# Optimization experiments

Measured on AMD Instinct MI355X. Metric: run time of the kernel, lower is better.

Reference implementation:

```python
import jax, jax.numpy as jnp
import numpy as np

N, E, IN_DIM, EDGE_DIM, EMB, H, L = 50000, 800000, 128, 32, 256, 8, 4
C = EMB // H  # per-head channels = 32
NEG_SLOPE = 0.2


def setup_inputs() -> dict:
    key = jax.random.key(0)
    ks = jax.random.split(key, 12)
    s = lambda d: 1.0 / np.sqrt(d)
    return {
        "x": jax.random.normal(ks[0], (N, IN_DIM), jnp.float32),
        "edge_index": jax.random.randint(ks[1], (2, E), 0, N, jnp.int32),
        "edge_attr": jax.random.normal(ks[2], (E, EDGE_DIM), jnp.float32),
        "w_in": jax.random.normal(ks[3], (IN_DIM, EMB), jnp.float32) * s(IN_DIM),
        "b_in": jnp.zeros((EMB,), jnp.float32),
        "W_l": jax.random.normal(ks[4], (L, EMB, EMB), jnp.float32) * s(EMB),
        "We_l": jax.random.normal(ks[5], (L, EDGE_DIM, EMB), jnp.float32) * s(EDGE_DIM),
        "att_src": jax.random.normal(ks[6], (L, H, C), jnp.float32) * s(C),
        "att_dst": jax.random.normal(ks[7], (L, H, C), jnp.float32) * s(C),
        "att_edge": jax.random.normal(ks[8], (L, H, C), jnp.float32) * s(C),
        "bias_l": jnp.zeros((L, EMB), jnp.float32),
        "w_out": jax.random.normal(ks[9], (EMB, 1), jnp.float32) * s(EMB),
        "b_out": jnp.zeros((1,), jnp.float32),
    }


def _gat_forward(x, edge_index, edge_attr, w_in, b_in, W_l, We_l,
                 att_src, att_dst, att_edge, bias_l, w_out, b_out):
    # add self loops (PyG GATConv default, edge_attr fill_value='mean')
    loop = jnp.arange(N, dtype=edge_index.dtype)
    src = jnp.concatenate([edge_index[0], loop])  # [E+N]
    dst = jnp.concatenate([edge_index[1], loop])
    ea = jnp.concatenate([edge_attr,
                          jnp.broadcast_to(edge_attr.mean(0), (N, EDGE_DIM))], 0)

    h = x @ w_in + b_in  # [N, EMB]
    for l in range(L):
        hp = (h @ W_l[l]).reshape(N, H, C)            # [N,H,C]
        ep = (ea @ We_l[l]).reshape(-1, H, C)         # [E+N,H,C]
        a_s = (hp * att_src[l]).sum(-1)               # [N,H]
        a_d = (hp * att_dst[l]).sum(-1)               # [N,H]
        e = a_s[src] + a_d[dst] + (ep * att_edge[l]).sum(-1)  # [E+N,H]
        e = jnp.where(e >= 0, e, NEG_SLOPE * e)
        # segment softmax over incoming edges of each dst node
        m = jax.ops.segment_max(e, dst, num_segments=N)
        e = jnp.exp(e - m[dst])
        denom = jax.ops.segment_sum(e, dst, num_segments=N)
        alpha = e / (denom[dst] + 1e-16)              # [E+N,H]
        msg = hp[src] * alpha[..., None]              # [E+N,H,C]
        h = jax.ops.segment_sum(msg, dst, num_segments=N).reshape(N, EMB) + bias_l[l]
    out = h @ w_out + b_out                           # [N,1]
    return out.squeeze(1)


def reference(x, edge_index, edge_attr, w_in, b_in, W_l, We_l,
              att_src, att_dst, att_edge, bias_l, w_out, b_out):
    return _gat_forward(x, edge_index, edge_attr, w_in, b_in, W_l, We_l,
                        att_src, att_dst, att_edge, bias_l, w_out, b_out)
```

## Files before the change

### kernel.cpp

```cpp
#include <hip/hip_runtime.h>

#define NN 50000
#define MPAD 50048
#define EE 800000
#define ETOT (EE + NN)
#define IN_DIM 128
#define EDGE_DIM 32
#define EMB 256
#define HH 8
#define LL 4
#define NEG_SLOPE 0.2f

typedef __attribute__((ext_vector_type(8))) short bf16x8;
typedef __attribute__((ext_vector_type(4))) float f32x4;

__device__ inline ushort f2bf_rn(float x) {
    union { float f; uint u; } v; v.f = x;
    uint r = v.u + 0x7FFFu + ((v.u >> 16) & 1u);
    return (ushort)(r >> 16);
}
__device__ inline float bf2f(ushort b) {
    union { uint u; float f; } v; v.u = ((uint)b) << 16;
    return v.f;
}

__device__ __forceinline__ void g2l16(const void* g, void* l) {
    __builtin_amdgcn_global_load_lds((const __attribute__((address_space(1))) void*)g,
                                     (__attribute__((address_space(3))) void*)l, 16, 0, 0);
}


__global__ void zero_int_kernel(int* p, int n) {
    int i = blockIdx.x * 256 + threadIdx.x;
    if (i < n) p[i] = 0;
}

__global__ void precompute_kernel(const float* __restrict__ We,
                                  const float* __restrict__ att_e,
                                  float* __restrict__ v) {
    int t = threadIdx.x;
    int l = t >> 8, rem = t & 255, d = rem >> 3, hh = rem & 7;
    float s = 0.f;
#pragma unroll
    for (int c = 0; c < 32; ++c)
        s += We[((size_t)(l * 32 + d)) * 256 + hh * 32 + c] * att_e[l * 256 + hh * 32 + c];
    v[t] = s;
}

__global__ __launch_bounds__(256) void col_partial(const float* __restrict__ ea,
                                                   float* __restrict__ part) {
    int t = threadIdx.x;
    int c = t & 7;
    int rg = t >> 3;
    float4 acc = {0.f, 0.f, 0.f, 0.f};
    for (int r = blockIdx.x * 32 + rg; r < EE; r += 1024 * 32) {
        float4 f = *(const float4*)&ea[(size_t)r * 32 + c * 4];
        acc.x += f.x; acc.y += f.y; acc.z += f.z; acc.w += f.w;
    }
    __shared__ float4 sm[256];
    sm[t] = acc;
    __syncthreads();
    for (int s = 16; s > 0; s >>= 1) {
        if (rg < s) {
            float4 o = sm[(rg + s) * 8 + c];
            float4 m = sm[t];
            m.x += o.x; m.y += o.y; m.z += o.z; m.w += o.w;
            sm[t] = m;
        }
        __syncthreads();
    }
    if (t < 8) *(float4*)&part[(size_t)blockIdx.x * 32 + t * 4] = sm[t];
}

__global__ __launch_bounds__(256) void col_final(const float* __restrict__ part,
                                                 float* __restrict__ mean_ea) {
    int t = threadIdx.x;
    int v = t & 31, c = t >> 5;
    float a0 = 0.f, a1 = 0.f, a2 = 0.f, a3 = 0.f;
    for (int b = c; b < 1024; b += 32) {
        a0 += part[(size_t)(b) * 32 + v];
        a1 += part[(size_t)(b + 8) * 32 + v];
        a2 += part[(size_t)(b + 16) * 32 + v];
        a3 += part[(size_t)(b + 24) * 32 + v];
    }
    float s = (a0 + a1) + (a2 + a3);
    __shared__ float sm[256];
    sm[t] = s;
    __syncthreads();
    if (c == 0) {
        float tot = 0.f;
#pragma unroll
        for (int k = 0; k < 8; ++k) tot += sm[k * 32 + v];
        mean_ea[v] = tot * (1.0f / EE);
    }
}

__global__ void hist_kernel(const int* __restrict__ ei, int* __restrict__ cnt) {
    int i = blockIdx.x * 256 + threadIdx.x;
    if (i >= ETOT) return;
    int dst = (i < EE) ? ei[EE + i] : (i - EE);
    atomicAdd(&cnt[dst], 1);
}

__global__ __launch_bounds__(256) void scan_phase1(const int* __restrict__ cnt,
                                                   int* __restrict__ bsum) {
    int b = blockIdx.x, t = threadIdx.x;
    int i0 = b * 1024 + t * 4;
    int s = 0;
#pragma unroll
    for (int r = 0; r < 4; ++r) s += (i0 + r < NN) ? cnt[i0 + r] : 0;
    for (int off = 1; off < 64; off <<= 1) s += __shfl_xor(s, off);
    __shared__ int wtot[4];
    if ((t & 63) == 0) wtot[t >> 6] = s;
    __syncthreads();
    if (t == 0) bsum[b] = wtot[0] + wtot[1] + wtot[2] + wtot[3];
}

__global__ void scan_phase2(int* __restrict__ bsum, int* __restrict__ row_ptr, int nb) {
    int lane = threadIdx.x;
    int vv = (lane < nb) ? bsum[lane] : 0;
    int incl = vv;
    for (int off = 1; off < 64; off <<= 1) {
        int u = __shfl_up(incl, off);
        if (lane >= off) incl += u;
    }
    if (lane < nb) bsum[lane] = incl - vv;
    if (lane == 0) row_ptr[NN] = ETOT;
}

__global__ __launch_bounds__(256) void scan_phase3(const int* __restrict__ cnt,
                                                   const int* __restrict__ bsum,
                                                   int* __restrict__ row_ptr,
                                                   int* __restrict__ fill) {
    int b = blockIdx.x, t = threadIdx.x;
    int i0 = b * 1024 + t * 4;
    int v[4];
    int s = 0;
#pragma unroll
    for (int r = 0; r < 4; ++r) { v[r] = (i0 + r < NN) ? cnt[i0 + r] : 0; s += v[r]; }
    int lane = t & 63, wv = t >> 6;
    int incl = s;
    for (int off = 1; off < 64; off <<= 1) {
        int u = __shfl_up(incl, off);
        if (lane >= off) incl += u;
    }
    __shared__ int wtot[4];
    if (lane == 63) wtot[wv] = incl;
    __syncthreads();
    int wpref = 0;
    for (int k = 0; k < wv; ++k) wpref += wtot[k];
    int start = bsum[b] + wpref + incl - s;
#pragma unroll
    for (int r = 0; r < 4; ++r) {
        int i = i0 + r;
        if (i < NN) { row_ptr[i] = start; fill[i] = start; }
        start += v[r];
    }
}

__global__ void scatter_kernel(const int* __restrict__ ei, int* __restrict__ fill,
                               int* __restrict__ sorted_src, int* __restrict__ sorted_eid) {
    int i = blockIdx.x * 256 + threadIdx.x;
    if (i >= ETOT) return;
    int dst, src;
    if (i < EE) { src = ei[i]; dst = ei[EE + i]; }
    else        { src = i - EE; dst = i - EE; }
    int pos = atomicAdd(&fill[dst], 1);
    sorted_src[pos] = src;
    sorted_eid[pos] = i;
}

__global__ __launch_bounds__(256) void split_weights(const float* __restrict__ w_in,
                                                     const float* __restrict__ W_l,
                                                     ushort* __restrict__ bh,
                                                     ushort* __restrict__ bl) {
    int t = blockIdx.x * 256 + threadIdx.x;
    if (t >= 32768 + 4 * 65536) return;
    float val;
    size_t dst;
    if (t < 32768) {
        int n = t >> 7, k = t & 127;
        val = w_in[(size_t)k * 256 + n];
        dst = (size_t)n * 128 + k;
    } else {
        int u = t - 32768;
        int l = u >> 16, r = u & 65535;
        int n = r >> 8, k = r & 255;
        val = W_l[(size_t)l * 65536 + (size_t)k * 256 + n];
        dst = 32768 + (size_t)l * 65536 + (size_t)n * 256 + k;
    }
    ushort hi = f2bf_rn(val);
    bh[dst] = hi;
    bl[dst] = f2bf_rn(val - bf2f(hi));
}

__global__ void split_x(const float* __restrict__ x, ushort* __restrict__ xh,
                        ushort* __restrict__ xl) {
    int i = blockIdx.x * 256 + threadIdx.x;
    if (i >= MPAD * 128) return;
    int n = i >> 7;
    float val = (n < NN) ? x[i] : 0.f;
    union { float f; uint u; } uv; uv.f = val;
    ushort hi = (ushort)(uv.u >> 16);
    xh[i] = hi;
    xl[i] = f2bf_rn(val - bf2f(hi));
}

__global__ __launch_bounds__(256) void edge_logits(const float* __restrict__ edge_attr,
                                                   const float* __restrict__ mean_ea,
                                                   const int* __restrict__ sorted_eid,
                                                   const float* __restrict__ v,
                                                   _Float16* __restrict__ e_all) {
    __shared__ float vs[1024];
    for (int t = threadIdx.x; t < 1024; t += 256) vs[t] = v[t];
    __syncthreads();
    int p = blockIdx.x * 256 + threadIdx.x;
    if (p >= ETOT) return;
    int eid = sorted_eid[p];
    const float4* row = (const float4*)((eid < EE) ? (edge_attr + (size_t)eid * 32) : mean_ea);
    float r[32];
#pragma unroll
    for (int q = 0; q < 8; ++q) {
        float4 f = row[q];
        r[q * 4] = f.x; r[q * 4 + 1] = f.y; r[q * 4 + 2] = f.z; r[q * 4 + 3] = f.w;
    }
    float acc[4][8] = {};
#pragma unroll 4
    for (int d = 0; d < 32; ++d) {
        float rv = r[d];
#pragma unroll
        for (int l = 0; l < 4; ++l)
#pragma unroll
            for (int h = 0; h < 8; ++h) acc[l][h] += rv * vs[l * 256 + d * 8 + h];
    }
#pragma unroll
    for (int l = 0; l < 4; ++l) {
        union { uint4 u; _Float16 h[8]; } pk;
#pragma unroll
        for (int h = 0; h < 8; ++h) pk.h[h] = (_Float16)acc[l][h];
        *(uint4*)&e_all[(size_t)l * ETOT * 8 + (size_t)p * 8] = pk.u;
    }
}

template <int MODE>
__global__ __launch_bounds__(256) void gemm_mfma(const ushort* __restrict__ Ah,
                                                 const ushort* __restrict__ Al,
                                                 const ushort* __restrict__ Bh,
                                                 const ushort* __restrict__ Bl,
                                                 const float* __restrict__ bias,
                                                 _Float16* __restrict__ hp_out,
                                                 ushort* __restrict__ hh_out,
                                                 ushort* __restrict__ hl_out,
                                                 int M, int K) {
    __shared__ __align__(16) ushort sAh[8192], sAl[8192], sBh[8192], sBl[8192];
    int tid = threadIdx.x;
    int m0 = blockIdx.x * 128, n0 = blockIdx.y * 128;
    int wid = tid >> 6, lane = tid & 63;
    int wm = wid & 1, wn = wid >> 1;
    int lr = lane & 15, grp = lane >> 4;
    f32x4 acc[4][4];
#pragma unroll
    for (int i = 0; i < 4; ++i)
#pragma unroll
        for (int j = 0; j < 4; ++j) acc[i][j] = (f32x4){0.f, 0.f, 0.f, 0.f};

    for (int k0 = 0; k0 < K; k0 += 64) {
        if (k0) __syncthreads();
#pragma unroll
        for (int i = 0; i < 4; ++i) {
            int ldso = wid * 2048 + i * 512;
            int o = ldso + lane * 8;
            int m = o >> 6;
            int kl = ((((o >> 3) & 7) ^ (m & 7)) << 3) + k0;
            size_t ga = (size_t)(m0 + m) * K + kl;
            size_t gb = (size_t)(n0 + m) * K + kl;
            g2l16(Ah + ga, sAh + ldso);
            g2l16(Al + ga, sAl + ldso);
            g2l16(Bh + gb, sBh + ldso);
            g2l16(Bl + gb, sBl + ldso);
        }
        __syncthreads();
#pragma unroll
        for (int ks = 0; ks < 2; ++ks) {
            bf16x8 vbh[4], vbl[4];
#pragma unroll
            for (int j = 0; j < 4; ++j) {
                int n = wn * 64 + j * 16 + lr;
                int off = n * 64 + ((ks * 32 + grp * 8) ^ ((n & 7) << 3));
                vbh[j] = *(const bf16x8*)&sBh[off];
                vbl[j] = *(const bf16x8*)&sBl[off];
            }
#pragma unroll
            for (int i = 0; i < 4; ++i) {
                int mm = wm * 64 + i * 16 + lr;
                int off = mm * 64 + ((ks * 32 + grp * 8) ^ ((mm & 7) << 3));
                bf16x8 vah = *(const bf16x8*)&sAh[off];
                bf16x8 valo = *(const bf16x8*)&sAl[off];
#pragma unroll
                for (int j = 0; j < 4; ++j) {
                    acc[i][j] = __builtin_amdgcn_mfma_f32_16x16x32_bf16(valo, vbh[j], acc[i][j], 0, 0, 0);
                    acc[i][j] = __builtin_amdgcn_mfma_f32_16x16x32_bf16(vah, vbl[j], acc[i][j], 0, 0, 0);
                    acc[i][j] = __builtin_amdgcn_mfma_f32_16x16x32_bf16(vah, vbh[j], acc[i][j], 0, 0, 0);
                }
            }
        }
    }
#pragma unroll
    for (int j = 0; j < 4; ++j) {
        int c = n0 + wn * 64 + j * 16 + lr;
        float bj = (MODE == 0) ? bias[c] : 0.f;
#pragma unroll
        for (int i = 0; i < 4; ++i) {
            int mb = m0 + wm * 64 + i * 16 + grp * 4;
#pragma unroll
            for (int r = 0; r < 4; ++r) {
                int row = mb + r;
                if (row < M) {
                    float val = acc[i][j][r] + bj;
                    if (MODE == 0) {
                        union { float f; uint u; } uv; uv.f = val;
                        ushort hi = (ushort)(uv.u >> 16);
                        hh_out[(size_t)row * 256 + c] = hi;
                        hl_out[(size_t)row * 256 + c] = f2bf_rn(val - bf2f(hi));
                    } else {
                        hp_out[(size_t)row * 256 + c] = (_Float16)val;
                    }
                }
            }
        }
    }
}


__global__ __launch_bounds__(256) void a_sd_kernel(const _Float16* __restrict__ hp,
                                                   const float* __restrict__ att_s,
                                                   const float* __restrict__ att_d,
                                                   float* __restrict__ a_s,
                                                   float* __restrict__ a_d) {
    int idx = blockIdx.x * 256 + threadIdx.x;
    if (idx >= NN * 8) return;
    int n = idx >> 3, hh = idx & 7;
    const uint4* base = (const uint4*)(hp + (size_t)n * 256 + hh * 32);
    const float4* as4 = (const float4*)(att_s + hh * 32);
    const float4* ad4 = (const float4*)(att_d + hh * 32);
    float ss = 0.f, sd = 0.f;
#pragma unroll
    for (int q = 0; q < 4; ++q) {
        union { uint4 u; _Float16 f[8]; } hv;
        hv.u = base[q];
        float4 s0 = as4[q * 2], s1 = as4[q * 2 + 1];
        float4 d0 = ad4[q * 2], d1 = ad4[q * 2 + 1];
        float f0 = (float)hv.f[0], f1 = (float)hv.f[1], f2 = (float)hv.f[2], f3 = (float)hv.f[3];
        float f4 = (float)hv.f[4], f5 = (float)hv.f[5], f6 = (float)hv.f[6], f7 = (float)hv.f[7];
        ss += f0 * s0.x + f1 * s0.y + f2 * s0.z + f3 * s0.w + f4 * s1.x + f5 * s1.y + f6 * s1.z + f7 * s1.w;
        sd += f0 * d0.x + f1 * d0.y + f2 * d0.z + f3 * d0.w + f4 * d1.x + f5 * d1.y + f6 * d1.z + f7 * d1.w;
    }
    a_s[idx] = ss;
    a_d[idx] = sd;
}

__global__ __launch_bounds__(256) void aggregate_kernel(const _Float16* __restrict__ hp,
                                                        const float* __restrict__ a_s,
                                                        const float* __restrict__ a_d,
                                                        const _Float16* __restrict__ e_l,
                                                        const int* __restrict__ sorted_src,
                                                        const int* __restrict__ row_ptr,
                                                        const float* __restrict__ bias,
                                                        ushort* __restrict__ h_hi,
                                                        ushort* __restrict__ h_lo) {
    int n = (blockIdx.x * 256 + threadIdx.x) >> 6;
    if (n >= NN) return;
    int lane = threadIdx.x & 63;
    int h1 = lane & 7;
    int eslot = lane >> 3;
    int h2 = lane >> 3;
    int beg = row_ptr[n], end = row_ptr[n + 1];
    float ad1 = a_d[n * 8 + h1];
    float ad2 = a_d[n * 8 + h2];
    float s = 0.f;
    float a0 = 0.f, a1 = 0.f, a2 = 0.f, a3 = 0.f;

    int deg = end - beg;
    int nfull = deg & ~7;
    for (int base = beg; base < beg + nfull; base += 8) {
        int j = base + eslot;
        int srce = sorted_src[j];
        float e = a_s[srce * 8 + h1] + ad1 + (float)e_l[(size_t)j * 8 + h1];
        e = (e >= 0.f) ? e : NEG_SLOPE * e;
        float w1 = __expf(e);
#pragma unroll
        for (int jj = 0; jj < 8; ++jj) {
            float w = __shfl(w1, jj * 8 + h2);
            int sj = __shfl(srce, jj * 8);
            union { uint2 u; _Float16 q[4]; } hv;
            hv.u = *(const uint2*)&hp[(size_t)sj * 256 + lane * 4];
            s += w;
            a0 += w * (float)hv.q[0];
            a1 += w * (float)hv.q[1];
            a2 += w * (float)hv.q[2];
            a3 += w * (float)hv.q[3];
        }
    }
    for (int j = beg + nfull; j < end; ++j) {
        int src = sorted_src[j];
        float e = a_s[src * 8 + h2] + ad2 + (float)e_l[(size_t)j * 8 + h2];
        e = (e >= 0.f) ? e : NEG_SLOPE * e;
        float w = __expf(e);
        union { uint2 u; _Float16 q[4]; } hv;
        hv.u = *(const uint2*)&hp[(size_t)src * 256 + lane * 4];
        s += w;
        a0 += w * (float)hv.q[0];
        a1 += w * (float)hv.q[1];
        a2 += w * (float)hv.q[2];
        a3 += w * (float)hv.q[3];
    }
    float inv = 1.0f / (s + 1e-16f);
    float4 b4 = *(const float4*)&bias[lane * 4];
    float o[4] = {a0 * inv + b4.x, a1 * inv + b4.y, a2 * inv + b4.z, a3 * inv + b4.w};
    ushort4 vhi, vlo;
    ushort* ph = (ushort*)&vhi;
    ushort* pl = (ushort*)&vlo;
#pragma unroll
    for (int c = 0; c < 4; ++c) {
        union { float f; uint u; } uv; uv.f = o[c];
        ph[c] = (ushort)(uv.u >> 16);
        pl[c] = f2bf_rn(o[c] - bf2f(ph[c]));
    }
    *(ushort4*)&h_hi[(size_t)n * 256 + lane * 4] = vhi;
    *(ushort4*)&h_lo[(size_t)n * 256 + lane * 4] = vlo;
}

__global__ __launch_bounds__(256) void out_kernel(const ushort* __restrict__ h_hi,
                                                  const ushort* __restrict__ h_lo,
                                                  const float* __restrict__ w_out,
                                                  const float* __restrict__ b_out,
                                                  float* __restrict__ out) {
    int n = (blockIdx.x * 256 + threadIdx.x) >> 6;
    if (n >= NN) return;
    int lane = threadIdx.x & 63;
    union { uint2 u; ushort s[4]; } uh, ul;
    uh.u = *(const uint2*)&h_hi[(size_t)n * 256 + lane * 4];
    ul.u = *(const uint2*)&h_lo[(size_t)n * 256 + lane * 4];
    const float4 wv = *(const float4*)&w_out[lane * 4];
    float s = (bf2f(uh.s[0]) + bf2f(ul.s[0])) * wv.x +
              (bf2f(uh.s[1]) + bf2f(ul.s[1])) * wv.y +
              (bf2f(uh.s[2]) + bf2f(ul.s[2])) * wv.z +
              (bf2f(uh.s[3]) + bf2f(ul.s[3])) * wv.w;
    for (int off = 1; off < 64; off <<= 1) s += __shfl_xor(s, off);
    if (lane == 0) out[n] = s + b_out[0];
}


extern "C" void kernel_launch(void* const* d_in, const int* in_sizes, int n_in,
                              void* d_out, int out_size, void* d_ws, size_t ws_size,
                              hipStream_t stream) {
    const float* x         = (const float*)d_in[0];
    const int*   edge_idx  = (const int*)d_in[1];
    const float* edge_attr = (const float*)d_in[2];
    const float* w_in      = (const float*)d_in[3];
    const float* b_in      = (const float*)d_in[4];
    const float* W_l       = (const float*)d_in[5];
    const float* We_l      = (const float*)d_in[6];
    const float* att_src   = (const float*)d_in[7];
    const float* att_dst   = (const float*)d_in[8];
    const float* att_edge  = (const float*)d_in[9];
    const float* bias_l    = (const float*)d_in[10];
    const float* w_out     = (const float*)d_in[11];
    const float* b_out     = (const float*)d_in[12];
    float* out = (float*)d_out;

    char* ws = (char*)d_ws;
    size_t off = 0;
    auto alloc = [&](size_t bytes) -> void* {
        void* p = ws + off;
        off = (off + bytes + 255) & ~(size_t)255;
        return p;
    };
    ushort*   h_hi       = (ushort*)alloc((size_t)MPAD * 256 * 2);
    ushort*   h_lo       = (ushort*)alloc((size_t)MPAD * 256 * 2);
    _Float16* hp16       = (_Float16*)alloc((size_t)MPAD * 256 * 2);
    float*    a_s        = (float*)alloc((size_t)NN * 8 * 4);
    float*    a_d        = (float*)alloc((size_t)NN * 8 * 4);
    int*      sorted_src = (int*)alloc((size_t)ETOT * 4);
    int*      sorted_eid = (int*)alloc((size_t)ETOT * 4);
    int*      row_ptr    = (int*)alloc((size_t)(NN + 1) * 4);
    int*      fill       = (int*)alloc((size_t)NN * 4);
    int*      cnt        = (int*)alloc((size_t)NN * 4);
    int*      bsum       = (int*)alloc(64 * 4);
    float*    col_part   = (float*)alloc((size_t)1024 * 32 * 4);
    float*    mean_ea    = (float*)alloc(32 * 4);
    float*    v          = (float*)alloc(1024 * 4);
    ushort*   bsp_hi     = (ushort*)alloc((size_t)294912 * 2);
    ushort*   bsp_lo     = (ushort*)alloc((size_t)294912 * 2);
    char*     uni        = (char*)alloc((size_t)4 * ETOT * 8 * 2);
    ushort*   xh         = (ushort*)uni;
    ushort*   xl         = (ushort*)(uni + (size_t)MPAD * 128 * 2);
    _Float16* e_all      = (_Float16*)uni;

    const int NB = (NN + 1023) / 1024;

    zero_int_kernel<<<(NN + 255) / 256, 256, 0, stream>>>(cnt, NN);
    precompute_kernel<<<1, 1024, 0, stream>>>(We_l, att_edge, v);
    col_partial<<<1024, 256, 0, stream>>>(edge_attr, col_part);
    col_final<<<1, 256, 0, stream>>>(col_part, mean_ea);
    split_weights<<<(294912 + 255) / 256, 256, 0, stream>>>(w_in, W_l, bsp_hi, bsp_lo);
    split_x<<<(MPAD * 128 + 255) / 256, 256, 0, stream>>>(x, xh, xl);

    dim3 ggrid((NN + 127) / 128, 2);
    gemm_mfma<0><<<ggrid, 256, 0, stream>>>(xh, xl, bsp_hi, bsp_lo, b_in,
                                            nullptr, h_hi, h_lo, NN, IN_DIM);

    hist_kernel<<<(ETOT + 255) / 256, 256, 0, stream>>>(edge_idx, cnt);
    scan_phase1<<<NB, 256, 0, stream>>>(cnt, bsum);
    scan_phase2<<<1, 64, 0, stream>>>(bsum, row_ptr, NB);
    scan_phase3<<<NB, 256, 0, stream>>>(cnt, bsum, row_ptr, fill);
    scatter_kernel<<<(ETOT + 255) / 256, 256, 0, stream>>>(edge_idx, fill, sorted_src, sorted_eid);
    edge_logits<<<(ETOT + 255) / 256, 256, 0, stream>>>(edge_attr, mean_ea, sorted_eid, v, e_all);

    for (int l = 0; l < LL; ++l) {
        const ushort* wh = bsp_hi + 32768 + (size_t)l * 65536;
        const ushort* wl = bsp_lo + 32768 + (size_t)l * 65536;
        gemm_mfma<1><<<ggrid, 256, 0, stream>>>(h_hi, h_lo, wh, wl, nullptr,
                                                hp16, nullptr, nullptr, NN, EMB);
        a_sd_kernel<<<(NN * 8 + 255) / 256, 256, 0, stream>>>(
            hp16, att_src + l * 256, att_dst + l * 256, a_s, a_d);
        aggregate_kernel<<<NN / 4, 256, 0, stream>>>(
            hp16, a_s, a_d, e_all + (size_t)l * ETOT * 8, sorted_src, row_ptr,
            bias_l + l * 256, h_hi, h_lo);
    }

    out_kernel<<<NN / 4, 256, 0, stream>>>(h_hi, h_lo, w_out, b_out, out);
}
```

Baseline: 725.7 us.

## Widen aggregate gathers to 16B, split edges across wave halves, drop tail loop

```diff
diff --git a/kernel.cpp b/kernel.cpp
--- a/kernel.cpp
+++ b/kernel.cpp
@@ -373,61 +373,71 @@
     int lane = threadIdx.x & 63;
     int h1 = lane & 7;
     int eslot = lane >> 3;
-    int h2 = lane >> 3;
+    int chan = lane & 31;
+    int half = lane >> 5;
+    int hh = chan >> 2;
     int beg = row_ptr[n], end = row_ptr[n + 1];
     float ad1 = a_d[n * 8 + h1];
-    float ad2 = a_d[n * 8 + h2];
     float s = 0.f;
-    float a0 = 0.f, a1 = 0.f, a2 = 0.f, a3 = 0.f;
-
-    int deg = end - beg;
-    int nfull = deg & ~7;
-    for (int base = beg; base < beg + nfull; base += 8) {
-        int j = base + eslot;
-        int srce = sorted_src[j];
-        float e = a_s[srce * 8 + h1] + ad1 + (float)e_l[(size_t)j * 8 + h1];
+    float acc[8] = {};
+
+    for (int base = beg; base < end; base += 8) {
+        int j8 = base + eslot;
+        bool valid = j8 < end;
+        int jc = valid ? j8 : (end - 1);
+        int srce = sorted_src[jc];
+        float e = a_s[srce * 8 + h1] + ad1 + (float)e_l[(size_t)jc * 8 + h1];
         e = (e >= 0.f) ? e : NEG_SLOPE * e;
-        float w1 = __expf(e);
-#pragma unroll
-        for (int jj = 0; jj < 8; ++jj) {
-            float w = __shfl(w1, jj * 8 + h2);
-            int sj = __shfl(srce, jj * 8);
-            union { uint2 u; _Float16 q[4]; } hv;
-            hv.u = *(const uint2*)&hp[(size_t)sj * 256 + lane * 4];
+        float w1 = valid ? __expf(e) : 0.f;
+        float wv[4];
+        int sv[4];
+#pragma unroll
+        for (int p = 0; p < 4; ++p) {
+            int slot = p * 2 + half;
+            wv[p] = __shfl(w1, slot * 8 + hh);
+            sv[p] = __shfl(srce, slot * 8);
+        }
+        union { uint4 u; _Float16 q[8]; } hv[4];
+#pragma unroll
+        for (int p = 0; p < 4; ++p)
+            hv[p].u = *(const uint4*)&hp[(size_t)sv[p] * 256 + chan * 8];
+#pragma unroll
+        for (int p = 0; p < 4; ++p) {
+            float w = wv[p];
             s += w;
-            a0 += w * (float)hv.q[0];
-            a1 += w * (float)hv.q[1];
-            a2 += w * (float)hv.q[2];
-            a3 += w * (float)hv.q[3];
-        }
-    }
-    for (int j = beg + nfull; j < end; ++j) {
-        int src = sorted_src[j];
-        float e = a_s[src * 8 + h2] + ad2 + (float)e_l[(size_t)j * 8 + h2];
-        e = (e >= 0.f) ? e : NEG_SLOPE * e;
-        float w = __expf(e);
-        union { uint2 u; _Float16 q[4]; } hv;
-        hv.u = *(const uint2*)&hp[(size_t)src * 256 + lane * 4];
-        s += w;
-        a0 += w * (float)hv.q[0];
-        a1 += w * (float)hv.q[1];
-        a2 += w * (float)hv.q[2];
-        a3 += w * (float)hv.q[3];
-    }
+#pragma unroll
+            for (int k = 0; k < 8; ++k) acc[k] += w * (float)hv[p].q[k];
+        }
+    }
+    s += __shfl_xor(s, 32);
+#pragma unroll
+    for (int k = 0; k < 8; ++k) acc[k] += __shfl_xor(acc[k], 32);
+
     float inv = 1.0f / (s + 1e-16f);
-    float4 b4 = *(const float4*)&bias[lane * 4];
-    float o[4] = {a0 * inv + b4.x, a1 * inv + b4.y, a2 * inv + b4.z, a3 * inv + b4.w};
-    ushort4 vhi, vlo;
-    ushort* ph = (ushort*)&vhi;
-    ushort* pl = (ushort*)&vlo;
-#pragma unroll
-    for (int c = 0; c < 4; ++c) {
-        union { float f; uint u; } uv; uv.f = o[c];
-        ph[c] = (ushort)(uv.u >> 16);
-        pl[c] = f2bf_rn(o[c] - bf2f(ph[c]));
-    }
-    *(ushort4*)&h_hi[(size_t)n * 256 + lane * 4] = vhi;
-    *(ushort4*)&h_lo[(size_t)n * 256 + lane * 4] = vlo;
+    const float4* b4 = (const float4*)&bias[chan * 8];
+    float4 bA = b4[0], bB = b4[1];
+    float o[8];
+    o[0] = acc[0] * inv + bA.x; o[1] = acc[1] * inv + bA.y;
+    o[2] = acc[2] * inv + bA.z; o[3] = acc[3] * inv + bA.w;
+    o[4] = acc[4] * inv + bB.x; o[5] = acc[5] * inv + bB.y;
+    o[6] = acc[6] * inv + bB.z; o[7] = acc[7] * inv + bB.w;
+    union { uint4 u; ushort v[8]; } pk;
+    if (half == 0) {
+#pragma unroll
+        for (int k = 0; k < 8; ++k) {
+            union { float f; uint u; } uv; uv.f = o[k];
+            pk.v[k] = (ushort)(uv.u >> 16);
+        }
+        *(uint4*)&h_hi[(size_t)n * 256 + chan * 8] = pk.u;
+    } else {
+#pragma unroll
+        for (int k = 0; k < 8; ++k) {
+            union { float f; uint u; } uv; uv.f = o[k];
+            ushort hi = (ushort)(uv.u >> 16);
+            pk.v[k] = f2bf_rn(o[k] - bf2f(hi));
+        }
+        *(uint4*)&h_lo[(size_t)n * 256 + chan * 8] = pk.u;
+    }
 }
 
 __global__ __launch_bounds__(256) void out_kernel(const ushort* __restrict__ h_hi,
```

Measured after the change: 723.9 us. No clear change (-0.3%).
